# Optimization experiments

Measured on AMD Instinct MI355X. Metric: run time of the kernel, lower is better.

## Reference

```python
import jax, jax.numpy as jnp
import numpy as np

NQ, NK, H, DH = 1024, 512, 8, 64


def setup_inputs() -> dict:
    key = jax.random.key(0)
    ks = jax.random.split(key, 8)
    b, n, d, g = 4, 4096, 1024, 4
    di = H * DH  # 512
    s = lambda fan: 1.0 / np.sqrt(fan)
    return {
        "x": jax.random.normal(ks[0], (b, n, d), jnp.float32),
        "w_qr": jax.random.normal(ks[1], (g, d), jnp.float32) * s(d),
        "w_kvr": jax.random.normal(ks[2], (g, d), jnp.float32) * s(d),
        "w_q": jax.random.normal(ks[3], (g, di, d), jnp.float32) * s(d),
        "w_kv": jax.random.normal(ks[4], (g, 2 * di, d), jnp.float32) * s(d),
        "w_out": jax.random.normal(ks[5], (g, d, di), jnp.float32) * s(di),
        "null_kv": jax.random.normal(ks[6], (2, g, H, 1, DH), jnp.float32),
        "null_token": jax.random.normal(ks[7], (1, 1, d), jnp.float32),
    }


def reference(x, w_qr, w_kvr, w_q, w_kv, w_out, null_kv, null_token):
    b, n, d = x.shape
    g = w_qr.shape[0]
    bidx = jnp.arange(b)[:, None, None]
    # --- routing: per-expert token scores, top-k select (router reference) ---
    q_logits = jnp.einsum("bnd,gd->bgn", x, w_qr)
    q_top, q_idx = jax.lax.top_k(q_logits, NQ)            # [b,g,NQ]
    q_scores = jax.nn.sigmoid(q_top)[..., None]           # [b,g,NQ,1]
    queries = x[bidx, q_idx]                              # [b,g,NQ,d]
    kv_logits = jnp.einsum("bnd,gd->bgn", x, w_kvr)
    kv_top, kv_idx = jax.lax.top_k(kv_logits, NK)
    kv_scores = jax.nn.sigmoid(kv_top)[:, :, None, :, None]  # [b,g,1,NK,1]
    key_values = x[bidx, kv_idx]                          # [b,g,NK,d]
    # --- grouped attention (1x1 grouped convs == per-group matmuls) ---
    q = jnp.einsum("bgnd,ged->bgne", queries, w_q)
    kv = jnp.einsum("bgnd,ged->bgne", key_values, w_kv)
    k, v = jnp.split(kv, 2, axis=-1)
    heads = lambda t: t.reshape(b, g, -1, H, DH).transpose(0, 1, 3, 2, 4)  # b g h n dh
    q, k, v = heads(q), heads(k), heads(v)
    v = v * kv_scores                                     # values_scale
    nk = jnp.broadcast_to(null_kv[0][None], (b, g, H, 1, DH))
    nv = jnp.broadcast_to(null_kv[1][None], (b, g, H, 1, DH))
    k = jnp.concatenate([nk, k], axis=-2)
    v = jnp.concatenate([nv, v], axis=-2)
    attn = jax.nn.softmax(jnp.einsum("bghid,bghjd->bghij", q, k) * DH ** -0.5, axis=-1)
    o = jnp.einsum("bghij,bghjd->bghid", attn, v)
    o = o.transpose(0, 1, 3, 2, 4).reshape(b, g, NQ, H * DH)
    o = jnp.einsum("bgne,gde->bgnd", o, w_out)
    o = o * q_scores
    # --- scatter-add back with count normalization ---
    flat_idx = q_idx.reshape(b, g * NQ)
    flat_o = o.reshape(b, g * NQ, d)
    b2 = jnp.arange(b)[:, None]
    summed = jnp.zeros_like(x).at[b2, flat_idx].add(flat_o)
    counts = jnp.zeros((b, n), x.dtype).at[b2, flat_idx].add(1.0)[..., None]
    meaned = summed / jnp.clip(counts, 1e-5)
    return jnp.where(counts > 0, meaned, null_token)
```

## Files before the change

kernel.cpp:

```cpp
#include <hip/hip_runtime.h>
#include <math.h>

#define NB 4
#define SEQ 4096
#define DM 1024
#define NG 4
#define DI 512
#define NQS 1024
#define NKS 512
#define NHD 8
#define DHD 64
#define VTS 520

typedef unsigned int u32;
typedef unsigned short u16;
typedef __bf16 bf16x8 __attribute__((ext_vector_type(8)));
typedef float f32x4 __attribute__((ext_vector_type(4)));

__device__ __forceinline__ float bf2f(u16 u) { return __uint_as_float(((u32)u) << 16); }
__device__ __forceinline__ u16 f2bf(float f) {
  u32 u = __float_as_uint(f);
  u32 r = (u + 0x7FFFu + ((u >> 16) & 1u)) >> 16;
  return (u16)r;
}
__device__ __forceinline__ u16 f2bfh(float f) {
  union { __bf16 b; u16 u; } cv;
  cv.b = (__bf16)f;
  return cv.u;
}

__global__ __launch_bounds__(256) void router_kernel(
    const float* __restrict__ x, const float* __restrict__ wqr,
    const float* __restrict__ wkvr, float* __restrict__ qlog,
    float* __restrict__ kvlog, u16* __restrict__ xbf,
    const float* __restrict__ wq, const float* __restrict__ wkv,
    const float* __restrict__ wout, u16* __restrict__ wqbf,
    u16* __restrict__ wkvbf, u16* __restrict__ woutbf) {
  __shared__ float wsm[8192];
  int tid = threadIdx.x;
  for (int k = tid; k < 8192; k += 256)
    wsm[k] = (k < 4096) ? wqr[k] : wkvr[k - 4096];

#pragma unroll
  for (int j = 0; j < 2; j++) {
    int idx = blockIdx.x * 512 + j * 256 + tid;
    const float* src; u16* dst; int off;
    if (idx < 524288)        { src = wq;   dst = wqbf;   off = idx; }
    else if (idx < 1572864)  { src = wkv;  dst = wkvbf;  off = idx - 524288; }
    else                     { src = wout; dst = woutbf; off = idx - 1572864; }
    float4 v = ((const float4*)src)[off];
    ushort4 o;
    o.x = f2bf(v.x); o.y = f2bf(v.y); o.z = f2bf(v.z); o.w = f2bf(v.w);
    ((ushort4*)dst)[off] = o;
  }
  __syncthreads();

  int widx = blockIdx.x * 4 + (tid >> 6);
  int lane = tid & 63;
  int b = widx >> 12, tok = widx & 4095;
  const float4* xr = (const float4*)(x + ((size_t)(b * SEQ + tok)) * DM);
  float4 xv[4];
#pragma unroll
  for (int i = 0; i < 4; i++) xv[i] = xr[i * 64 + lane];
  ushort4* xrow = (ushort4*)(xbf + ((size_t)(b * SEQ + tok)) * DM);
#pragma unroll
  for (int i = 0; i < 4; i++) {
    ushort4 o;
    o.x = f2bf(xv[i].x); o.y = f2bf(xv[i].y);
    o.z = f2bf(xv[i].z); o.w = f2bf(xv[i].w);
    xrow[i * 64 + lane] = o;
  }
  float accs[8];
#pragma unroll
  for (int r = 0; r < 8; r++) {
    const float4* wr = (const float4*)(wsm + r * 1024);
    float a = 0.f;
#pragma unroll
    for (int i = 0; i < 4; i++) {
      float4 w4 = wr[i * 64 + lane];
      a += xv[i].x * w4.x + xv[i].y * w4.y + xv[i].z * w4.z + xv[i].w * w4.w;
    }
    accs[r] = a;
  }
#pragma unroll
  for (int r = 0; r < 8; r++) {
    float a = accs[r];
#pragma unroll
    for (int off = 32; off >= 1; off >>= 1) a += __shfl_xor(a, off);
    if (lane == 0) {
      if (r < 4) qlog[((b << 2) | r) * SEQ + tok] = a;
      else kvlog[((b << 2) | (r - 4)) * SEQ + tok] = a;
    }
  }
}

__global__ __launch_bounds__(256) void topk_kernel(
    const float* __restrict__ qlog, const float* __restrict__ kvlog,
    int* __restrict__ qidx, float* __restrict__ qscore,
    int* __restrict__ kvidx, float* __restrict__ kvscore) {
  __shared__ u32 keys[4096];
  __shared__ int eqlist[2048];
  __shared__ int scnt[4];
  __shared__ int s_gt, s_eq;
  int which = blockIdx.x >> 4;
  int bg = blockIdx.x & 15;
  int K = (which == 0) ? NQS : NKS;
  const float* L = ((which == 0) ? qlog : kvlog) + bg * 4096;
  int* out_idx = ((which == 0) ? qidx : kvidx) + bg * K;
  float* out_score = ((which == 0) ? qscore : kvscore) + bg * K;
  int tid = threadIdx.x;
  for (int e = tid; e < 4096; e += 256) {
    u32 u = __float_as_uint(L[e]);
    keys[e] = (u >> 31) ? ~u : (u | 0x80000000u);
  }
  if (tid == 0) { s_gt = 0; s_eq = 0; }
  __syncthreads();
  u32 prefix = 0;
  int remaining = K;
  for (int bit = 31; bit >= 0; --bit) {
    u32 want = prefix | (1u << bit);
    u32 mask = ~((1u << bit) - 1u);
    int c = 0;
    for (int e = tid; e < 4096; e += 256) c += ((keys[e] & mask) == want) ? 1 : 0;
#pragma unroll
    for (int off = 32; off >= 1; off >>= 1) c += __shfl_xor(c, off);
    if ((tid & 63) == 0) scnt[tid >> 6] = c;
    __syncthreads();
    int total = scnt[0] + scnt[1] + scnt[2] + scnt[3];
    if (total >= remaining) prefix = want;
    else remaining -= total;
    __syncthreads();
  }
  u32 T = prefix;
  for (int e = tid; e < 4096; e += 256) {
    u32 k = keys[e];
    if (k > T) {
      int pos = atomicAdd(&s_gt, 1);
      out_idx[pos] = e;
      float v = L[e];
      out_score[pos] = 1.0f / (1.0f + __expf(-v));
    } else if (k == T) {
      int p = atomicAdd(&s_eq, 1);
      if (p < 2048) eqlist[p] = e;
    }
  }
  __syncthreads();
  int gt = s_gt;
  int eq = min(s_eq, 2048);
  int need = K - gt;
  for (int i = tid; i < eq; i += 256) {
    int my = eqlist[i];
    int rank = 0;
    for (int j = 0; j < eq; j++) rank += (eqlist[j] < my) ? 1 : 0;
    if (rank < need) {
      int pos = gt + rank;
      out_idx[pos] = my;
      float v = L[my];
      out_score[pos] = 1.0f / (1.0f + __expf(-v));
    }
  }
}

__global__ __launch_bounds__(256) void qpos_build(const int* __restrict__ qidx,
                                                  int* __restrict__ qpos) {
  int bg = blockIdx.x;
  int tid = threadIdx.x;
  int* base = qpos + bg * 4096;
  for (int i = tid; i < 4096; i += 256) base[i] = -1;
  __syncthreads();
  for (int p = tid; p < NQS; p += 256) base[qidx[bg * NQS + p]] = p;
}

struct Ptr4 { const u16* p[4]; };

__device__ __forceinline__ void mfma_core(Ptr4 A, Ptr4 B, u16* Asm, u16* Bsm,
                                          int ktiles, int tid, f32x4 (&acc)[4][4]) {
  int w = tid >> 6, lane = tid & 63;
  int col = lane & 15, quad = lane >> 4;
  int wr = w >> 1, wc = w & 1;
  for (int kt = 0; kt < ktiles; kt++) {
#pragma unroll
    for (int r = 0; r < 4; r++) {
      char* ldsA = (char*)Asm + (r * 256 + w * 64) * 16;
      __builtin_amdgcn_global_load_lds(
          (const __attribute__((address_space(1))) void*)(A.p[r] + kt * 64),
          (__attribute__((address_space(3))) void*)ldsA, 16, 0, 0);
    }
#pragma unroll
    for (int r = 0; r < 4; r++) {
      char* ldsB = (char*)Bsm + (r * 256 + w * 64) * 16;
      __builtin_amdgcn_global_load_lds(
          (const __attribute__((address_space(1))) void*)(B.p[r] + kt * 64),
          (__attribute__((address_space(3))) void*)ldsB, 16, 0, 0);
    }
    __syncthreads();
#pragma unroll
    for (int k04 = 0; k04 < 8; k04 += 4) {
      bf16x8 af[4], bfr[4];
#pragma unroll
      for (int t = 0; t < 4; t++) {
        int rowa = wr * 64 + t * 16 + col;
        int sp = (quad + k04) ^ (col & 7);
        af[t] = *(const bf16x8*)((const char*)Asm + (rowa * 8 + sp) * 16);
        int rowb = wc * 64 + t * 16 + col;
        bfr[t] = *(const bf16x8*)((const char*)Bsm + (rowb * 8 + sp) * 16);
      }
#pragma unroll
      for (int t = 0; t < 4; t++)
#pragma unroll
        for (int u = 0; u < 4; u++)
          acc[t][u] = __builtin_amdgcn_mfma_f32_16x16x32_bf16(af[t], bfr[u], acc[t][u], 0, 0, 0);
    }
    __syncthreads();
  }
}

__global__ __launch_bounds__(256) void gemm_qkvproj(
    const u16* __restrict__ xbf, const int* __restrict__ qidx,
    const int* __restrict__ kvidx, const u16* __restrict__ wqbf,
    const u16* __restrict__ wkvbf, const float* __restrict__ kvscore,
    u16* __restrict__ qbuf, u16* __restrict__ kbuf, u16* __restrict__ vtbuf) {
  __shared__ __align__(16) u16 Asm[8192], Bsm[8192];
  __shared__ int ridx[128];
  int tid = threadIdx.x;
  int grp = blockIdx.x & 7;
  int local = blockIdx.x >> 3;
  bool is_q = grp < 4;
  int g = grp & 3;
  int b = local >> 5, r5 = local & 31;
  int bg = (b << 2) | g;
  int w = tid >> 6, lane = tid & 63;
  int col = lane & 15, quad = lane >> 4;
  int wr = w >> 1, wc = w & 1;

  if (is_q) {
    int col0 = (r5 & 3) * 128, row0 = (r5 >> 2) * 128;
    if (tid < 128) ridx[tid] = qidx[bg * NQS + row0 + tid];
    __syncthreads();
    Ptr4 A, B;
#pragma unroll
    for (int r = 0; r < 4; r++) {
      int G = r * 256 + tid;
      int row = G >> 3;
      int seg = (G & 7) ^ (row & 7);
      A.p[r] = xbf + ((size_t)b * SEQ + ridx[row]) * DM + seg * 8;
      B.p[r] = wqbf + ((size_t)g * DI + col0 + row) * DM + seg * 8;
    }
    f32x4 acc[4][4] = {};
    mfma_core(A, B, Asm, Bsm, DM / 64, tid, acc);
#pragma unroll
    for (int t = 0; t < 4; t++)
#pragma unroll
      for (int u = 0; u < 4; u++)
#pragma unroll
        for (int r = 0; r < 4; r++) {
          int rowg = row0 + wr * 64 + t * 16 + quad * 4 + r;
          int colg = col0 + wc * 64 + u * 16 + col;
          qbuf[((size_t)bg * NQS + rowg) * DI + colg] = f2bf(acc[t][u][r] * 0.125f);
        }
  } else {
    int col0 = (r5 & 7) * 128, row0 = (r5 >> 3) * 128;
    if (tid < 128) ridx[tid] = kvidx[bg * NKS + row0 + tid];
    __syncthreads();
    Ptr4 A, B;
#pragma unroll
    for (int r = 0; r < 4; r++) {
      int G = r * 256 + tid;
      int row = G >> 3;
      int seg = (G & 7) ^ (row & 7);
      A.p[r] = xbf + ((size_t)b * SEQ + ridx[row]) * DM + seg * 8;
      B.p[r] = wkvbf + ((size_t)g * (2 * DI) + col0 + row) * DM + seg * 8;
    }
    f32x4 acc[4][4] = {};
    mfma_core(A, B, Asm, Bsm, DM / 64, tid, acc);
    if (col0 < DI) {
#pragma unroll
      for (int t = 0; t < 4; t++)
#pragma unroll
        for (int u = 0; u < 4; u++)
#pragma unroll
          for (int r = 0; r < 4; r++) {
            int rowg = row0 + wr * 64 + t * 16 + quad * 4 + r;
            int colg = col0 + wc * 64 + u * 16 + col;
            kbuf[((size_t)bg * NKS + rowg) * DI + colg] = f2bf(acc[t][u][r]);
          }
    } else {
#pragma unroll
      for (int t = 0; t < 4; t++)
#pragma unroll
        for (int r = 0; r < 4; r++) {
          int rowg = row0 + wr * 64 + t * 16 + quad * 4 + r;
          float sc = kvscore[bg * NKS + rowg];
#pragma unroll
          for (int u = 0; u < 4; u++) {
            int vc = col0 - DI + wc * 64 + u * 16 + col;
            int h = vc >> 6, d = vc & 63;
            vtbuf[(((size_t)bg * NHD + h) * DHD + d) * VTS + rowg] =
                f2bf(acc[t][u][r] * sc);
          }
        }
    }
  }
}

__global__ __launch_bounds__(256) void gemm_outproj(
    const u16* __restrict__ obuf, const u16* __restrict__ woutbf,
    const float* __restrict__ qscore, float* __restrict__ oproj, int bgbase) {
  int z = blockIdx.z, bg = bgbase + z, g = bg & 3;
  int row0 = blockIdx.y * 128, col0 = blockIdx.x * 128;
  __shared__ __align__(16) u16 Asm[8192], Bsm[8192];
  int tid = threadIdx.x;
  Ptr4 A, B;
#pragma unroll
  for (int r = 0; r < 4; r++) {
    int G = r * 256 + tid;
    int row = G >> 3;
    int seg = (G & 7) ^ (row & 7);
    A.p[r] = obuf + ((size_t)bg * NQS + row0 + row) * DI + seg * 8;
    B.p[r] = woutbf + ((size_t)g * DM + col0 + row) * DI + seg * 8;
  }
  f32x4 acc[4][4] = {};
  mfma_core(A, B, Asm, Bsm, DI / 64, tid, acc);
  int w = tid >> 6, lane = tid & 63;
  int col = lane & 15, quad = lane >> 4;
  int wr = w >> 1, wc = w & 1;
  float* obase = oproj + (size_t)z * NQS * DM;
#pragma unroll
  for (int t = 0; t < 4; t++)
#pragma unroll
    for (int r = 0; r < 4; r++) {
      int rowg = row0 + wr * 64 + t * 16 + quad * 4 + r;
      float sc = qscore[bg * NQS + rowg];
      float* orow = obase + (size_t)rowg * DM;
#pragma unroll
      for (int u = 0; u < 4; u++) {
        int colg = col0 + wc * 64 + u * 16 + col;
        orow[colg] = acc[t][u][r] * sc;
      }
    }
}

__global__ __launch_bounds__(256) void finalize_gather(
    const float* __restrict__ oproj, const int* __restrict__ qpos,
    const float* __restrict__ null_token, float* __restrict__ dout, int b0) {
  int blk = blockIdx.x;
  int b = b0 + (blk >> 12);
  int tok = blk & 4095;
  int tid = threadIdx.x;
  float4 acc = {0.f, 0.f, 0.f, 0.f};
  int cnt = 0;
#pragma unroll
  for (int g = 0; g < 4; g++) {
    int pos = qpos[(((b << 2) | g)) * 4096 + tok];
    if (pos >= 0) {
      const float4* row =
          (const float4*)(oproj + (((size_t)((b - b0) * 4 + g)) * NQS + pos) * DM);
      float4 v = row[tid];
      acc.x += v.x; acc.y += v.y; acc.z += v.z; acc.w += v.w;
      cnt++;
    }
  }
  float4* dst = (float4*)(dout + ((size_t)b * SEQ + tok) * DM) + tid;
  if (cnt > 0) {
    float inv = 1.0f / cnt;
    acc.x *= inv; acc.y *= inv; acc.z *= inv; acc.w *= inv;
    *dst = acc;
  } else {
    *dst = ((const float4*)null_token)[tid];
  }
}

__global__ __launch_bounds__(256, 4) void attn_mfma(
    const u16* __restrict__ qbuf, const u16* __restrict__ kbuf,
    const u16* __restrict__ vtbuf, const float* __restrict__ null_kv,
    u16* __restrict__ obuf) {
  int qt = blockIdx.x;
  int h = blockIdx.y;
  int bg = blockIdx.z;
  int g = bg & 3;
  int tid = threadIdx.x;
  int w = tid >> 6, lane = tid & 63;
  int col = lane & 15, quad = lane >> 4;

  __shared__ __align__(16) u16 Ks[64][72];
  __shared__ __align__(16) u16 Vts[64][72];
  __shared__ __align__(16) u16 Ps[4][32][72];

  int q0 = qt * 128 + w * 32;
  const u16* qp0 = qbuf + ((size_t)bg * NQS + q0 + col) * DI + h * DHD + quad * 8;
  bf16x8 qa[2][2];
  qa[0][0] = *(const bf16x8*)qp0;
  qa[0][1] = *(const bf16x8*)(qp0 + 32);
  qa[1][0] = *(const bf16x8*)(qp0 + 16 * DI);
  qa[1][1] = *(const bf16x8*)(qp0 + 16 * DI + 32);

  const float* kn = null_kv + ((size_t)(0 * NG + g) * NHD + h) * DHD;
  const float* vn = null_kv + ((size_t)(1 * NG + g) * NHD + h) * DHD;
  float m_run[2], l_lane[2];
  f32x4 oacc[2][4];
#pragma unroll
  for (int s = 0; s < 2; s++) {
    float sn = 0.f;
#pragma unroll
    for (int i = 0; i < 8; i++) {
      sn += (float)qa[s][0][i] * kn[quad * 8 + i];
      sn += (float)qa[s][1][i] * kn[32 + quad * 8 + i];
    }
    sn += __shfl_xor(sn, 16);
    sn += __shfl_xor(sn, 32);
    m_run[s] = sn;
    l_lane[s] = (quad == 0) ? 1.f : 0.f;
  }
#pragma unroll
  for (int t = 0; t < 4; t++) {
    float v = vn[t * 16 + col];
    f32x4 tmp = {v, v, v, v};
    oacc[0][t] = tmp;
    oacc[1][t] = tmp;
  }

  int sr = tid >> 2, ss = tid & 3;
  const u16* kptr = kbuf + ((size_t)bg * NKS + sr) * DI + h * DHD + ss * 16;
  const u16* vptr = vtbuf + (((size_t)bg * NHD + h) * DHD + sr) * VTS + ss * 16;
  uint4* kdst = (uint4*)&Ks[sr][ss * 16];
  uint4* vdst = (uint4*)&Vts[sr][ss * 16];
  uint4 ck0, ck1, cv0, cv1;
  { const uint4* p = (const uint4*)kptr; ck0 = p[0]; ck1 = p[1]; }
  { const uint4* p = (const uint4*)vptr; cv0 = p[0]; cv1 = p[1]; }

  for (int c = 0; c < 8; ++c) {
    kdst[0] = ck0; kdst[1] = ck1;
    vdst[0] = cv0; vdst[1] = cv1;
    if (c < 7) {
      const uint4* p = (const uint4*)(kptr + (size_t)(c + 1) * 64 * DI);
      ck0 = p[0]; ck1 = p[1];
      const uint4* q4 = (const uint4*)(vptr + (c + 1) * 64);
      cv0 = q4[0]; cv1 = q4[1];
    }
    __syncthreads();

    f32x4 sv[2][4];
#pragma unroll
    for (int t = 0; t < 4; t++) {
      bf16x8 kb0 = *(const bf16x8*)&Ks[t * 16 + col][quad * 8];
      bf16x8 kb1 = *(const bf16x8*)&Ks[t * 16 + col][quad * 8 + 32];
      f32x4 z = {0.f, 0.f, 0.f, 0.f};
      f32x4 s0 = __builtin_amdgcn_mfma_f32_16x16x32_bf16(kb0, qa[0][0], z, 0, 0, 0);
      sv[0][t] = __builtin_amdgcn_mfma_f32_16x16x32_bf16(kb1, qa[0][1], s0, 0, 0, 0);
      f32x4 s1 = __builtin_amdgcn_mfma_f32_16x16x32_bf16(kb0, qa[1][0], z, 0, 0, 0);
      sv[1][t] = __builtin_amdgcn_mfma_f32_16x16x32_bf16(kb1, qa[1][1], s1, 0, 0, 0);
    }

#pragma unroll
    for (int s = 0; s < 2; s++) {
      float pm = sv[s][0][0];
#pragma unroll
      for (int t = 0; t < 4; t++)
#pragma unroll
        for (int r = 0; r < 4; r++) pm = fmaxf(pm, sv[s][t][r]);
      pm = fmaxf(pm, __shfl_xor(pm, 16));
      pm = fmaxf(pm, __shfl_xor(pm, 32));
      if (!__all(pm <= m_run[s] + 8.0f)) {
        float mnew = fmaxf(m_run[s], pm);
        float alpha = __expf(m_run[s] - mnew);
        m_run[s] = mnew;
        l_lane[s] *= alpha;
#pragma unroll
        for (int r = 0; r < 4; r++) {
          float a_o = __shfl(alpha, quad * 4 + r);
#pragma unroll
          for (int t = 0; t < 4; t++) oacc[s][t][r] *= a_o;
        }
      }
      float rs = 0.f;
#pragma unroll
      for (int t = 0; t < 4; t++) {
        float p0 = __expf(sv[s][t][0] - m_run[s]);
        float p1 = __expf(sv[s][t][1] - m_run[s]);
        float p2 = __expf(sv[s][t][2] - m_run[s]);
        float p3 = __expf(sv[s][t][3] - m_run[s]);
        rs += (p0 + p1) + (p2 + p3);
        u32 lo = (u32)f2bfh(p0) | ((u32)f2bfh(p1) << 16);
        u32 hi = (u32)f2bfh(p2) | ((u32)f2bfh(p3) << 16);
        *(uint2*)&Ps[w][s * 16 + col][t * 16 + quad * 4] = make_uint2(lo, hi);
      }
      l_lane[s] += rs;
    }

#pragma unroll
    for (int s2 = 0; s2 < 2; s2++) {
      bf16x8 pa0 = *(const bf16x8*)&Ps[w][col][s2 * 32 + quad * 8];
      bf16x8 pa1 = *(const bf16x8*)&Ps[w][16 + col][s2 * 32 + quad * 8];
#pragma unroll
      for (int t = 0; t < 4; t++) {
        bf16x8 vb = *(const bf16x8*)&Vts[t * 16 + col][s2 * 32 + quad * 8];
        oacc[0][t] = __builtin_amdgcn_mfma_f32_16x16x32_bf16(pa0, vb, oacc[0][t], 0, 0, 0);
        oacc[1][t] = __builtin_amdgcn_mfma_f32_16x16x32_bf16(pa1, vb, oacc[1][t], 0, 0, 0);
      }
    }
    __syncthreads();
  }

#pragma unroll
  for (int s = 0; s < 2; s++) {
    float l = l_lane[s];
    l += __shfl_xor(l, 16);
    l += __shfl_xor(l, 32);
    float inv = 1.0f / l;
#pragma unroll
    for (int r = 0; r < 4; r++) {
      float ir = __shfl(inv, quad * 4 + r);
#pragma unroll
      for (int t = 0; t < 4; t++) {
        obuf[((size_t)bg * NQS + q0 + s * 16 + quad * 4 + r) * DI + h * DHD +
             t * 16 + col] = f2bfh(oacc[s][t][r] * ir);
      }
    }
  }
}

extern "C" void kernel_launch(void* const* d_in, const int* in_sizes, int n_in,
                              void* d_out, int out_size, void* d_ws, size_t ws_size,
                              hipStream_t stream) {
  const float* x = (const float*)d_in[0];
  const float* wqr = (const float*)d_in[1];
  const float* wkvr = (const float*)d_in[2];
  const float* wq = (const float*)d_in[3];
  const float* wkv = (const float*)d_in[4];
  const float* wout = (const float*)d_in[5];
  const float* nullkv = (const float*)d_in[6];
  const float* nulltok = (const float*)d_in[7];
  float* out = (float*)d_out;
  char* ws = (char*)d_ws;
  float* qlog = (float*)(ws + 0);
  float* kvlog = (float*)(ws + 262144);
  int* qidx = (int*)(ws + 524288);
  int* kvidx = (int*)(ws + 589824);
  float* qscore = (float*)(ws + 622592);
  float* kvscore = (float*)(ws + 688128);
  u16* qbuf = (u16*)(ws + 786432);
  u16* kbuf = (u16*)(ws + 17563648);
  u16* vtbuf = (u16*)(ws + 25952256);
  u16* obuf = (u16*)(ws + 34476032);
  u16* xbf = (u16*)(ws + 51253248);
  u16* wqbf = (u16*)(ws + 84807680);
  u16* wkvbf = (u16*)(ws + 89001984);
  u16* woutbf = (u16*)(ws + 97390592);
  int* qpos = (int*)(ws + 0);
  float* oproj = (float*)(ws + 51253248);

  router_kernel<<<4096, 256, 0, stream>>>(x, wqr, wkvr, qlog, kvlog, xbf, wq,
                                          wkv, wout, wqbf, wkvbf, woutbf);
  topk_kernel<<<32, 256, 0, stream>>>(qlog, kvlog, qidx, qscore, kvidx, kvscore);
  qpos_build<<<16, 256, 0, stream>>>(qidx, qpos);
  gemm_qkvproj<<<1024, 256, 0, stream>>>(xbf, qidx, kvidx, wqbf, wkvbf, kvscore,
                                         qbuf, kbuf, vtbuf);
  attn_mfma<<<dim3(8, 8, 16), 256, 0, stream>>>(qbuf, kbuf, vtbuf, nullkv, obuf);
  gemm_outproj<<<dim3(8, 8, 8), 256, 0, stream>>>(obuf, woutbf, qscore, oproj, 0);
  finalize_gather<<<8192, 256, 0, stream>>>(oproj, qpos, nulltok, out, 0);
  gemm_outproj<<<dim3(8, 8, 8), 256, 0, stream>>>(obuf, woutbf, qscore, oproj, 8);
  finalize_gather<<<8192, 256, 0, stream>>>(oproj, qpos, nulltok, out, 2);
}
```

Baseline: 339.4 us.

## Fuse qpos build into top-k and merge split outproj/finalize launches

```diff
diff --git a/kernel.cpp b/kernel.cpp
--- a/kernel.cpp
+++ b/kernel.cpp
@@ -36,11 +36,7 @@
     const float* __restrict__ wq, const float* __restrict__ wkv,
     const float* __restrict__ wout, u16* __restrict__ wqbf,
     u16* __restrict__ wkvbf, u16* __restrict__ woutbf) {
-  __shared__ float wsm[8192];
   int tid = threadIdx.x;
-  for (int k = tid; k < 8192; k += 256)
-    wsm[k] = (k < 4096) ? wqr[k] : wkvr[k - 4096];
-
 #pragma unroll
   for (int j = 0; j < 2; j++) {
     int idx = blockIdx.x * 512 + j * 256 + tid;
@@ -53,7 +49,6 @@
     o.x = f2bf(v.x); o.y = f2bf(v.y); o.z = f2bf(v.z); o.w = f2bf(v.w);
     ((ushort4*)dst)[off] = o;
   }
-  __syncthreads();
 
   int widx = blockIdx.x * 4 + (tid >> 6);
   int lane = tid & 63;
@@ -73,7 +68,8 @@
   float accs[8];
 #pragma unroll
   for (int r = 0; r < 8; r++) {
-    const float4* wr = (const float4*)(wsm + r * 1024);
+    const float4* wr =
+        (const float4*)(r < 4 ? wqr + (r << 10) : wkvr + ((r - 4) << 10));
     float a = 0.f;
 #pragma unroll
     for (int i = 0; i < 4; i++) {
@@ -97,7 +93,8 @@
 __global__ __launch_bounds__(256) void topk_kernel(
     const float* __restrict__ qlog, const float* __restrict__ kvlog,
     int* __restrict__ qidx, float* __restrict__ qscore,
-    int* __restrict__ kvidx, float* __restrict__ kvscore) {
+    int* __restrict__ kvidx, float* __restrict__ kvscore,
+    int* __restrict__ qpos) {
   __shared__ u32 keys[4096];
   __shared__ int eqlist[2048];
   __shared__ int scnt[4];
@@ -108,11 +105,14 @@
   const float* L = ((which == 0) ? qlog : kvlog) + bg * 4096;
   int* out_idx = ((which == 0) ? qidx : kvidx) + bg * K;
   float* out_score = ((which == 0) ? qscore : kvscore) + bg * K;
+  int* qposb = qpos + bg * 4096;
   int tid = threadIdx.x;
   for (int e = tid; e < 4096; e += 256) {
     u32 u = __float_as_uint(L[e]);
     keys[e] = (u >> 31) ? ~u : (u | 0x80000000u);
   }
+  if (which == 0)
+    for (int e = tid; e < 4096; e += 256) qposb[e] = -1;
   if (tid == 0) { s_gt = 0; s_eq = 0; }
   __syncthreads();
   u32 prefix = 0;
@@ -137,8 +137,10 @@
     if (k > T) {
       int pos = atomicAdd(&s_gt, 1);
       out_idx[pos] = e;
-      float v = L[e];
+      u32 uo = (k >> 31) ? (k & 0x7FFFFFFFu) : ~k;
+      float v = __uint_as_float(uo);
       out_score[pos] = 1.0f / (1.0f + __expf(-v));
+      if (which == 0) qposb[e] = pos;
     } else if (k == T) {
       int p = atomicAdd(&s_eq, 1);
       if (p < 2048) eqlist[p] = e;
@@ -155,20 +157,13 @@
     if (rank < need) {
       int pos = gt + rank;
       out_idx[pos] = my;
-      float v = L[my];
+      u32 k2 = keys[my];
+      u32 uo = (k2 >> 31) ? (k2 & 0x7FFFFFFFu) : ~k2;
+      float v = __uint_as_float(uo);
       out_score[pos] = 1.0f / (1.0f + __expf(-v));
-    }
-  }
-}
-
-__global__ __launch_bounds__(256) void qpos_build(const int* __restrict__ qidx,
-                                                  int* __restrict__ qpos) {
-  int bg = blockIdx.x;
-  int tid = threadIdx.x;
-  int* base = qpos + bg * 4096;
-  for (int i = tid; i < 4096; i += 256) base[i] = -1;
-  __syncthreads();
-  for (int p = tid; p < NQS; p += 256) base[qidx[bg * NQS + p]] = p;
+      if (which == 0) qposb[my] = pos;
+    }
+  }
 }
 
 struct Ptr4 { const u16* p[4]; };
@@ -223,12 +218,11 @@
   __shared__ __align__(16) u16 Asm[8192], Bsm[8192];
   __shared__ int ridx[128];
   int tid = threadIdx.x;
-  int grp = blockIdx.x & 7;
-  int local = blockIdx.x >> 3;
-  bool is_q = grp < 4;
-  int g = grp & 3;
-  int b = local >> 5, r5 = local & 31;
-  int bg = (b << 2) | g;
+  int id = blockIdx.x;
+  bool is_q = (id & 1) == 0;
+  int sid = id >> 1;
+  int bg = sid >> 5, r5 = sid & 31;
+  int b = bg >> 2, g = bg & 3;
   int w = tid >> 6, lane = tid & 63;
   int col = lane & 15, quad = lane >> 4;
   int wr = w >> 1, wc = w & 1;
@@ -305,8 +299,9 @@
 
 __global__ __launch_bounds__(256) void gemm_outproj(
     const u16* __restrict__ obuf, const u16* __restrict__ woutbf,
-    const float* __restrict__ qscore, float* __restrict__ oproj, int bgbase) {
-  int z = blockIdx.z, bg = bgbase + z, g = bg & 3;
+    const float* __restrict__ qscore, float* __restrict__ oproj_lo,
+    float* __restrict__ oproj_hi) {
+  int bg = blockIdx.z, g = bg & 3;
   int row0 = blockIdx.y * 128, col0 = blockIdx.x * 128;
   __shared__ __align__(16) u16 Asm[8192], Bsm[8192];
   int tid = threadIdx.x;
@@ -324,7 +319,7 @@
   int w = tid >> 6, lane = tid & 63;
   int col = lane & 15, quad = lane >> 4;
   int wr = w >> 1, wc = w & 1;
-  float* obase = oproj + (size_t)z * NQS * DM;
+  float* obase = (bg < 8 ? oproj_lo : oproj_hi) + (size_t)(bg & 7) * NQS * DM;
 #pragma unroll
   for (int t = 0; t < 4; t++)
 #pragma unroll
@@ -341,12 +336,15 @@
 }
 
 __global__ __launch_bounds__(256) void finalize_gather(
-    const float* __restrict__ oproj, const int* __restrict__ qpos,
-    const float* __restrict__ null_token, float* __restrict__ dout, int b0) {
+    const float* __restrict__ oproj_lo, const float* __restrict__ oproj_hi,
+    const int* __restrict__ qpos, const float* __restrict__ null_token,
+    float* __restrict__ dout) {
   int blk = blockIdx.x;
-  int b = b0 + (blk >> 12);
+  int b = blk >> 12;
   int tok = blk & 4095;
   int tid = threadIdx.x;
+  const float* obase = (b < 2) ? oproj_lo : oproj_hi;
+  int zoff = (b & 1) * 4;
   float4 acc = {0.f, 0.f, 0.f, 0.f};
   int cnt = 0;
 #pragma unroll
@@ -354,7 +352,7 @@
     int pos = qpos[(((b << 2) | g)) * 4096 + tok];
     if (pos >= 0) {
       const float4* row =
-          (const float4*)(oproj + (((size_t)((b - b0) * 4 + g)) * NQS + pos) * DM);
+          (const float4*)(obase + ((size_t)(zoff + g) * NQS + pos) * DM);
       float4 v = row[tid];
       acc.x += v.x; acc.y += v.y; acc.z += v.z; acc.w += v.w;
       cnt++;
@@ -547,17 +545,18 @@
   u16* wkvbf = (u16*)(ws + 89001984);
   u16* woutbf = (u16*)(ws + 97390592);
   int* qpos = (int*)(ws + 0);
-  float* oproj = (float*)(ws + 51253248);
+  float* oproj_lo = (float*)(ws + 786432);
+  float* oproj_hi = (float*)(ws + 51253248);
 
   router_kernel<<<4096, 256, 0, stream>>>(x, wqr, wkvr, qlog, kvlog, xbf, wq,
                                           wkv, wout, wqbf, wkvbf, woutbf);
-  topk_kernel<<<32, 256, 0, stream>>>(qlog, kvlog, qidx, qscore, kvidx, kvscore);
-  qpos_build<<<16, 256, 0, stream>>>(qidx, qpos);
+  topk_kernel<<<32, 256, 0, stream>>>(qlog, kvlog, qidx, qscore, kvidx, kvscore,
+                                      qpos);
   gemm_qkvproj<<<1024, 256, 0, stream>>>(xbf, qidx, kvidx, wqbf, wkvbf, kvscore,
                                          qbuf, kbuf, vtbuf);
   attn_mfma<<<dim3(8, 8, 16), 256, 0, stream>>>(qbuf, kbuf, vtbuf, nullkv, obuf);
-  gemm_outproj<<<dim3(8, 8, 8), 256, 0, stream>>>(obuf, woutbf, qscore, oproj, 0);
-  finalize_gather<<<8192, 256, 0, stream>>>(oproj, qpos, nulltok, out, 0);
-  gemm_outproj<<<dim3(8, 8, 8), 256, 0, stream>>>(obuf, woutbf, qscore, oproj, 8);
-  finalize_gather<<<8192, 256, 0, stream>>>(oproj, qpos, nulltok, out, 2);
-}
+  gemm_outproj<<<dim3(8, 8, 16), 256, 0, stream>>>(obuf, woutbf, qscore,
+                                                   oproj_lo, oproj_hi);
+  finalize_gather<<<16384, 256, 0, stream>>>(oproj_lo, oproj_hi, qpos, nulltok,
+                                             out);
+}
```

Measured after the change: 330.0 us. -2.8%, faster.
